# Optimization experiments

Hardware: AMD Instinct MI355X
Metric: run time of the kernel (lower is better)

## Reference

```python
import jax, jax.numpy as jnp
import numpy as np

B, T, C, H = 4096, 128, 128, 64  # T must equal BLOCK_SIZE=128, C=EMBEDDING_DIM=128


def setup_inputs() -> dict:
    key = jax.random.key(0)
    k1, k2, k3, k4, k5, k6 = jax.random.split(key, 6)
    source_embedding = jax.random.normal(k1, (B, T, C), dtype=jnp.float32)
    target_embedding = jax.random.normal(k2, (B, T, C), dtype=jnp.float32)
    # realistic padding: positions < length are valid; guarantees col 0 valid (no NaN rows)
    lengths = jax.random.randint(k3, (B,), 1, T + 1)
    pad_mask = jnp.arange(T)[None, :] < lengths[:, None]  # (B, T) bool
    Wq = jax.random.normal(k4, (C, H), dtype=jnp.float32) * 0.02
    Wk = jax.random.normal(k5, (C, H), dtype=jnp.float32) * 0.02
    Wv = jax.random.normal(k6, (C, H), dtype=jnp.float32) * 0.02
    return {"source_embedding": source_embedding, "target_embedding": target_embedding,
            "pad_mask": pad_mask, "Wq": Wq, "Wk": Wk, "Wv": Wv}


def reference(source_embedding, target_embedding, pad_mask, Wq, Wk, Wv):
    # q from target, k/v from source (cross-attention capable), bias-free projections
    q = target_embedding @ Wq   # (B, T, H)
    k = source_embedding @ Wk   # (B, T, H)
    v = source_embedding @ Wv   # (B, T, H)
    scale = k.shape[-1] ** -0.5
    wei = jnp.einsum('btd,bsd->bts', q, k) * scale  # (B, T, T)
    causal = jnp.tril(jnp.ones((T, T), dtype=bool))  # needs_future_mask=True
    mask = pad_mask[:, None, :] & causal[None, :, :]  # fuse pad + future masks
    wei = jnp.where(mask, wei, -jnp.inf)
    wei = jax.nn.softmax(wei, axis=-1)
    # dropout disabled (eval mode) for deterministic reference
    out = wei @ v  # (B, T, H)
    return out
```

## Files before the change

kernel.cpp:

```cpp
#include <hip/hip_runtime.h>
#include <stdint.h>


typedef uint32_t u32x2 __attribute__((ext_vector_type(2)));
typedef uint32_t u32x4 __attribute__((ext_vector_type(4)));
typedef float    f32x4 __attribute__((ext_vector_type(4)));
typedef __bf16   bf16x8 __attribute__((ext_vector_type(8)));

static __device__ __forceinline__ uint32_t pack2(float a, float b) {
  uint32_t ua = __builtin_bit_cast(uint32_t, a);
  uint32_t ub = __builtin_bit_cast(uint32_t, b);
  ua += 0x7FFFu + ((ua >> 16) & 1u);
  ub += 0x7FFFu + ((ub >> 16) & 1u);
  return (ua >> 16) | (ub & 0xFFFF0000u);
}
static __device__ __forceinline__ f32x4 mfma16(u32x4 a, u32x4 b, f32x4 c) {
  return __builtin_amdgcn_mfma_f32_16x16x32_bf16(
      __builtin_bit_cast(bf16x8, a), __builtin_bit_cast(bf16x8, b), c, 0, 0, 0);
}

__global__ void prep_w(const float* __restrict__ Wq, const float* __restrict__ Wk,
                       const float* __restrict__ Wv, const void* __restrict__ mask,
                       uint32_t* __restrict__ ws) {
  const int blk = blockIdx.x;
  const int l = threadIdx.x;
  if (blk < 48) {
    const int m  = blk >> 4;
    const int ct = (blk >> 2) & 3;
    const int ks = blk & 3;
    const float* W = (m == 0) ? Wq : ((m == 1) ? Wk : Wv);
    const int h  = ct * 16 + (l & 15);
    const int c0 = ks * 32 + (l >> 4) * 8;
    u32x4 v;
#pragma unroll
    for (int p = 0; p < 4; ++p)
      v[p] = pack2(W[(c0 + 2 * p) * 64 + h], W[(c0 + 2 * p + 1) * 64 + h]);
    ((u32x4*)ws)[blk * 64 + l] = v;
  } else {
    const uint32_t* mw = (const uint32_t*)mask;
    int fl = 0;
    for (int i = l * 16; i < l * 16 + 16; ++i) {
      uint32_t x = mw[i];
      if (x == 0x3F800000u) fl = 2;
      else if (x > 1u && fl != 2) fl = 1;
    }
#pragma unroll
    for (int off = 32; off > 0; off >>= 1) {
      int o = __shfl_down(fl, off);
      fl = (o > fl) ? o : fl;
    }
    if (l == 0) ws[12288] = (uint32_t)fl;
  }
}

__global__ __launch_bounds__(512, 4) void attn_fused(
    const float* __restrict__ src, const float* __restrict__ tgt,
    const void* __restrict__ mask, const uint32_t* __restrict__ ws,
    float* __restrict__ out) {
  __shared__ __align__(16) uint8_t lds[66048];
  uint8_t* const EMB = lds;
  uint8_t* const Qb  = lds + 16384;
  uint8_t* const Kb  = lds + 32768;
  uint8_t* const Vb  = lds + 49152;
  float*  const BIAS = (float*)(lds + 65536);

  const int b   = blockIdx.x;
  const int tid = (int)threadIdx.x;
  const int l   = tid & 63;
  const int w   = tid >> 6;
  const int l15 = l & 15;
  const int g4  = l >> 4;
  const int ct  = w & 3;
  const int sg  = (w >> 2) * 2;

  const u32x4* wsv = (const u32x4*)ws;
  const int mflag = (int)ws[12288];
  const float* const srcb = src + (size_t)b * 16384;
  const float* const tgtb = tgt + (size_t)b * 16384;

  u32x4 wk[4], wv[4], wq[4];
#pragma unroll
  for (int ks = 0; ks < 4; ++ks) {
    wk[ks] = wsv[((4 + ct) * 4 + ks) * 64 + l];
    wv[ks] = wsv[((8 + ct) * 4 + ks) * 64 + l];
  }

  f32x4 pf[4];
  auto stage_load = [&](const float* gbase) {
#pragma unroll
    for (int p = 0; p < 4; ++p)
      pf[p] = *(const f32x4*)(gbase + tid * 4 + p * 2048);
  };
  auto stage_write = [&]() {
#pragma unroll
    for (int p = 0; p < 4; ++p) {
      const int c   = tid + p * 512;
      const int row = c >> 5;
      const int cc  = c & 31;
      u32x2 d = { pack2(pf[p][0], pf[p][1]), pack2(pf[p][2], pf[p][3]) };
      *(u32x2*)(EMB + (row << 8) + ((((cc >> 1) ^ (row & 7))) << 4) + ((cc & 1) << 3)) = d;
    }
  };

  auto projKV = [&](int half) {
#pragma unroll
    for (int i = 0; i < 2; ++i) {
      const int st  = sg + i;
      const int row = st * 16 + l15;
      f32x4 cK = {0, 0, 0, 0}, cV = {0, 0, 0, 0};
#pragma unroll
      for (int ks = 0; ks < 4; ++ks) {
        u32x4 e = *(const u32x4*)(EMB + (row << 8) + ((((ks * 4 + g4) ^ (row & 7))) << 4));
        cK = mfma16(wk[ks], e, cK);
        cV = mfma16(e, wv[ks], cV);
      }
      const int s  = half * 64 + st * 16 + l15;
      const int h0 = ct * 16 + g4 * 4;
      u32x2 dk = { pack2(cK[0], cK[1]), pack2(cK[2], cK[3]) };
      *(u32x2*)(Kb + (s << 7) + ((((h0 >> 3) ^ (s & 7))) << 4) + ((h0 & 7) << 1)) = dk;
      const int s0 = half * 64 + st * 16 + g4 * 4;
      const int h  = ct * 16 + l15;
      u32x2 dv = { pack2(cV[0], cV[1]), pack2(cV[2], cV[3]) };
      *(u32x2*)(Vb + (h << 8) + ((((s0 >> 3) ^ (h & 7))) << 4) + ((s0 & 7) << 1)) = dv;
    }
  };
  auto projQ = [&](int half) {
#pragma unroll
    for (int i = 0; i < 2; ++i) {
      const int st  = sg + i;
      const int row = st * 16 + l15;
      f32x4 cQ = {0, 0, 0, 0};
#pragma unroll
      for (int ks = 0; ks < 4; ++ks) {
        u32x4 e = *(const u32x4*)(EMB + (row << 8) + ((((ks * 4 + g4) ^ (row & 7))) << 4));
        cQ = mfma16(wq[ks], e, cQ);
      }
      const int t  = half * 64 + st * 16 + l15;
      const int h0 = ct * 16 + g4 * 4;
      u32x2 dq = { pack2(cQ[0], cQ[1]), pack2(cQ[2], cQ[3]) };
      *(u32x2*)(Qb + (t << 7) + ((((h0 >> 3) ^ (t & 7))) << 4) + ((h0 & 7) << 1)) = dq;
    }
  };

  stage_load(srcb);
  float biasv = 0.0f;
  if (tid < 128) {
    bool valid;
    if (mflag == 1)      valid = ((const uint8_t*)mask)[b * 128 + tid] != 0;
    else if (mflag == 0) valid = ((const int*)mask)[b * 128 + tid] != 0;
    else                 valid = ((const float*)mask)[b * 128 + tid] != 0.0f;
    biasv = valid ? 0.0f : -1e30f;
  }
  stage_write();
  if (tid < 128) BIAS[tid] = biasv;
  __syncthreads();
  stage_load(srcb + 8192);
  projKV(0);
  __syncthreads();
  stage_write();
  __syncthreads();
  stage_load(tgtb);
  projKV(1);
#pragma unroll
  for (int ks = 0; ks < 4; ++ks)
    wq[ks] = wsv[(ct * 4 + ks) * 64 + l];
  __syncthreads();
  stage_write();
  __syncthreads();
  stage_load(tgtb + 8192);
  projQ(0);
  __syncthreads();
  stage_write();
  __syncthreads();
  projQ(1);
  __syncthreads();

  const int tq = 16 * w + l15;
  u32x4 qf0 = *(const u32x4*)(Qb + (tq << 7) + (((g4 ^ (tq & 7))) << 4));
  u32x4 qf1 = *(const u32x4*)(Qb + (tq << 7) + ((((4 + g4) ^ (tq & 7))) << 4));

  f32x4 sacc[8];
#pragma unroll
  for (int mt = 0; mt < 8; ++mt) sacc[mt] = {0, 0, 0, 0};
#pragma unroll
  for (int mt = 0; mt < 8; ++mt) {
    const int srow = mt * 16 + l15;
    u32x4 k0 = *(const u32x4*)(Kb + (srow << 7) + (((g4 ^ (srow & 7))) << 4));
    u32x4 k1 = *(const u32x4*)(Kb + (srow << 7) + ((((4 + g4) ^ (srow & 7))) << 4));
    sacc[mt] = mfma16(k0, qf0, sacc[mt]);
    sacc[mt] = mfma16(k1, qf1, sacc[mt]);
  }

  float m = -3.0e38f;
#pragma unroll
  for (int mt = 0; mt < 8; ++mt) {
    f32x4 b4 = *(const f32x4*)(BIAS + mt * 16 + g4 * 4);
#pragma unroll
    for (int r = 0; r < 4; ++r) {
      float v = sacc[mt][r] * 0.125f + b4[r];
      sacc[mt][r] = v;
      m = fmaxf(m, v);
    }
  }
  m = fmaxf(m, __shfl_xor(m, 16));
  m = fmaxf(m, __shfl_xor(m, 32));
  float sum = 0.0f;
#pragma unroll
  for (int mt = 0; mt < 8; ++mt) {
#pragma unroll
    for (int r = 0; r < 4; ++r) {
      const int s = mt * 16 + g4 * 4 + r;
      float p = __expf(sacc[mt][r] - m);
      p = (s <= tq) ? p : 0.0f;
      sacc[mt][r] = p;
      sum += p;
    }
  }
  sum += __shfl_xor(sum, 16);
  sum += __shfl_xor(sum, 32);
  const float inv = 1.0f / sum;

  uint8_t* const Pr = (l15 < 8) ? (EMB + w * 2048 + l15 * 256)
                                : (Qb + w * 2048 + (l15 - 8) * 256);
#pragma unroll
  for (int mt = 0; mt < 8; ++mt) {
    u32x2 d = { pack2(sacc[mt][0], sacc[mt][1]), pack2(sacc[mt][2], sacc[mt][3]) };
    const int c = mt * 2 + (g4 >> 1);
    *(u32x2*)(Pr + (((c ^ l15)) << 4) + ((g4 & 1) << 3)) = d;
  }
  __syncthreads();

  f32x4 oacc[4];
#pragma unroll
  for (int vt = 0; vt < 4; ++vt) oacc[vt] = {0, 0, 0, 0};
#pragma unroll
  for (int ks = 0; ks < 4; ++ks) {
    u32x4 pb = *(const u32x4*)(Pr + ((((ks * 4 + g4) ^ l15)) << 4));
#pragma unroll
    for (int vt = 0; vt < 4; ++vt) {
      const int vrow = vt * 16 + l15;
      u32x4 vf = *(const u32x4*)(Vb + (vrow << 8) + ((((ks * 4 + g4) ^ (vrow & 7))) << 4));
      oacc[vt] = mfma16(vf, pb, oacc[vt]);
    }
  }

  float* const ob = out + (size_t)b * 8192 + (size_t)tq * 64;
#pragma unroll
  for (int vt = 0; vt < 4; ++vt) {
    f32x4 o = { oacc[vt][0] * inv, oacc[vt][1] * inv,
                oacc[vt][2] * inv, oacc[vt][3] * inv };
    *(f32x4*)(ob + vt * 16 + g4 * 4) = o;
  }
}

extern "C" void kernel_launch(void* const* d_in, const int* in_sizes, int n_in,
                              void* d_out, int out_size, void* d_ws, size_t ws_size,
                              hipStream_t stream) {
  const float* src = (const float*)d_in[0];
  const float* tgt = (const float*)d_in[1];
  const void*  msk = d_in[2];
  const float* Wq  = (const float*)d_in[3];
  const float* Wk  = (const float*)d_in[4];
  const float* Wv  = (const float*)d_in[5];
  uint32_t* ws = (uint32_t*)d_ws;
  float* out = (float*)d_out;
  const int B = in_sizes[0] / (128 * 128);

  hipLaunchKernelGGL(prep_w, dim3(49), dim3(64), 0, stream, Wq, Wk, Wv, msk, ws);
  hipLaunchKernelGGL(attn_fused, dim3(B), dim3(512), 0, stream,
                     src, tgt, msk, ws, out);
}
```

Measured before the change: 144.8 us.

## Keep Q and P in registers via lane shuffles, drop Q LDS buffer

Each wave now projects Q for its own 16 query rows entirely in registers and feeds it to QK^T through cross-lane shuffles instead of staging it in an LDS buffer. The softmax probabilities are likewise rearranged with shuffles rather than written to LDS, which removes one barrier and the Q buffer. LDS per block drops from about 66KB to about 49KB, and launch bounds are raised so more blocks can be resident per CU. s_setprio is also wrapped around the MFMA loops. In exchange there are many more shuffle instructions, and the higher occupancy target may force register spills.

```diff
diff --git a/kernel.cpp b/kernel.cpp
--- a/kernel.cpp
+++ b/kernel.cpp
@@ -53,16 +53,15 @@
   }
 }
 
-__global__ __launch_bounds__(512, 4) void attn_fused(
+__global__ __launch_bounds__(512, 6) void attn_fused(
     const float* __restrict__ src, const float* __restrict__ tgt,
     const void* __restrict__ mask, const uint32_t* __restrict__ ws,
     float* __restrict__ out) {
-  __shared__ __align__(16) uint8_t lds[66048];
+  __shared__ __align__(16) uint8_t lds[49664];
   uint8_t* const EMB = lds;
-  uint8_t* const Qb  = lds + 16384;
-  uint8_t* const Kb  = lds + 32768;
-  uint8_t* const Vb  = lds + 49152;
-  float*  const BIAS = (float*)(lds + 65536);
+  uint8_t* const Kb  = lds + 16384;
+  uint8_t* const Vb  = lds + 32768;
+  float*  const BIAS = (float*)(lds + 49152);
 
   const int b   = blockIdx.x;
   const int tid = (int)threadIdx.x;
@@ -78,7 +77,7 @@
   const float* const srcb = src + (size_t)b * 16384;
   const float* const tgtb = tgt + (size_t)b * 16384;
 
-  u32x4 wk[4], wv[4], wq[4];
+  u32x4 wk[4], wv[4];
 #pragma unroll
   for (int ks = 0; ks < 4; ++ks) {
     wk[ks] = wsv[((4 + ct) * 4 + ks) * 64 + l];
@@ -124,22 +123,23 @@
       *(u32x2*)(Vb + (h << 8) + ((((s0 >> 3) ^ (h & 7))) << 4) + ((s0 & 7) << 1)) = dv;
     }
   };
-  auto projQ = [&](int half) {
-#pragma unroll
-    for (int i = 0; i < 2; ++i) {
-      const int st  = sg + i;
-      const int row = st * 16 + l15;
-      f32x4 cQ = {0, 0, 0, 0};
-#pragma unroll
-      for (int ks = 0; ks < 4; ++ks) {
-        u32x4 e = *(const u32x4*)(EMB + (row << 8) + ((((ks * 4 + g4) ^ (row & 7))) << 4));
-        cQ = mfma16(wq[ks], e, cQ);
-      }
-      const int t  = half * 64 + st * 16 + l15;
-      const int h0 = ct * 16 + g4 * 4;
-      u32x2 dq = { pack2(cQ[0], cQ[1]), pack2(cQ[2], cQ[3]) };
-      *(u32x2*)(Qb + (t << 7) + ((((h0 >> 3) ^ (t & 7))) << 4) + ((h0 & 7) << 1)) = dq;
-    }
+
+  uint32_t qp[8];
+  auto projQ_own = [&]() {
+    const int row = (w & 3) * 16 + l15;
+    f32x4 c0 = {0,0,0,0}, c1 = {0,0,0,0}, c2 = {0,0,0,0}, c3 = {0,0,0,0};
+#pragma unroll
+    for (int ks = 0; ks < 4; ++ks) {
+      u32x4 e = *(const u32x4*)(EMB + (row << 8) + ((((ks * 4 + g4) ^ (row & 7))) << 4));
+      c0 = mfma16(wsv[(0  + ks) * 64 + l], e, c0);
+      c1 = mfma16(wsv[(4  + ks) * 64 + l], e, c1);
+      c2 = mfma16(wsv[(8  + ks) * 64 + l], e, c2);
+      c3 = mfma16(wsv[(12 + ks) * 64 + l], e, c3);
+    }
+    qp[0] = pack2(c0[0], c0[1]); qp[1] = pack2(c0[2], c0[3]);
+    qp[2] = pack2(c1[0], c1[1]); qp[3] = pack2(c1[2], c1[3]);
+    qp[4] = pack2(c2[0], c2[1]); qp[5] = pack2(c2[2], c2[3]);
+    qp[6] = pack2(c3[0], c3[1]); qp[7] = pack2(c3[2], c3[3]);
   };
 
   stage_load(srcb);
@@ -161,35 +161,51 @@
   __syncthreads();
   stage_load(tgtb);
   projKV(1);
-#pragma unroll
-  for (int ks = 0; ks < 4; ++ks)
-    wq[ks] = wsv[(ct * 4 + ks) * 64 + l];
   __syncthreads();
   stage_write();
   __syncthreads();
   stage_load(tgtb + 8192);
-  projQ(0);
-  __syncthreads();
-  stage_write();
-  __syncthreads();
-  projQ(1);
-  __syncthreads();
+  if (w < 4) projQ_own();
+  __syncthreads();
+  stage_write();
+  __syncthreads();
+  if (w >= 4) projQ_own();
+
+  const int hi2 = g4 >> 1;
+  const int sA  = ((g4 & 1) * 2) * 16 + l15;
+  const int sB  = sA + 16;
+
+  u32x4 qB[2];
+#pragma unroll
+  for (int ks = 0; ks < 2; ++ks) {
+    uint32_t a0 = (uint32_t)__shfl((int)qp[4 * ks + 0], sA);
+    uint32_t a1 = (uint32_t)__shfl((int)qp[4 * ks + 1], sA);
+    uint32_t a2 = (uint32_t)__shfl((int)qp[4 * ks + 2], sA);
+    uint32_t a3 = (uint32_t)__shfl((int)qp[4 * ks + 3], sA);
+    uint32_t b0 = (uint32_t)__shfl((int)qp[4 * ks + 0], sB);
+    uint32_t b1 = (uint32_t)__shfl((int)qp[4 * ks + 1], sB);
+    uint32_t b2 = (uint32_t)__shfl((int)qp[4 * ks + 2], sB);
+    uint32_t b3 = (uint32_t)__shfl((int)qp[4 * ks + 3], sB);
+    qB[ks][0] = hi2 ? a2 : a0;
+    qB[ks][1] = hi2 ? a3 : a1;
+    qB[ks][2] = hi2 ? b2 : b0;
+    qB[ks][3] = hi2 ? b3 : b1;
+  }
 
   const int tq = 16 * w + l15;
-  u32x4 qf0 = *(const u32x4*)(Qb + (tq << 7) + (((g4 ^ (tq & 7))) << 4));
-  u32x4 qf1 = *(const u32x4*)(Qb + (tq << 7) + ((((4 + g4) ^ (tq & 7))) << 4));
-
   f32x4 sacc[8];
 #pragma unroll
   for (int mt = 0; mt < 8; ++mt) sacc[mt] = {0, 0, 0, 0};
+  __builtin_amdgcn_s_setprio(1);
 #pragma unroll
   for (int mt = 0; mt < 8; ++mt) {
     const int srow = mt * 16 + l15;
     u32x4 k0 = *(const u32x4*)(Kb + (srow << 7) + (((g4 ^ (srow & 7))) << 4));
     u32x4 k1 = *(const u32x4*)(Kb + (srow << 7) + ((((4 + g4) ^ (srow & 7))) << 4));
-    sacc[mt] = mfma16(k0, qf0, sacc[mt]);
-    sacc[mt] = mfma16(k1, qf1, sacc[mt]);
-  }
+    sacc[mt] = mfma16(k0, qB[0], sacc[mt]);
+    sacc[mt] = mfma16(k1, qB[1], sacc[mt]);
+  }
+  __builtin_amdgcn_s_setprio(0);
 
   float m = -3.0e38f;
 #pragma unroll
@@ -220,22 +236,32 @@
   sum += __shfl_xor(sum, 32);
   const float inv = 1.0f / sum;
 
-  uint8_t* const Pr = (l15 < 8) ? (EMB + w * 2048 + l15 * 256)
-                                : (Qb + w * 2048 + (l15 - 8) * 256);
-#pragma unroll
-  for (int mt = 0; mt < 8; ++mt) {
-    u32x2 d = { pack2(sacc[mt][0], sacc[mt][1]), pack2(sacc[mt][2], sacc[mt][3]) };
-    const int c = mt * 2 + (g4 >> 1);
-    *(u32x2*)(Pr + (((c ^ l15)) << 4) + ((g4 & 1) << 3)) = d;
-  }
-  __syncthreads();
+  uint32_t sp[16];
+#pragma unroll
+  for (int mt = 0; mt < 8; ++mt) {
+    sp[2 * mt]     = pack2(sacc[mt][0], sacc[mt][1]);
+    sp[2 * mt + 1] = pack2(sacc[mt][2], sacc[mt][3]);
+  }
 
   f32x4 oacc[4];
 #pragma unroll
   for (int vt = 0; vt < 4; ++vt) oacc[vt] = {0, 0, 0, 0};
+  __builtin_amdgcn_s_setprio(1);
 #pragma unroll
   for (int ks = 0; ks < 4; ++ks) {
-    u32x4 pb = *(const u32x4*)(Pr + ((((ks * 4 + g4) ^ l15)) << 4));
+    uint32_t a0 = (uint32_t)__shfl((int)sp[4 * ks + 0], sA);
+    uint32_t a1 = (uint32_t)__shfl((int)sp[4 * ks + 1], sA);
+    uint32_t a2 = (uint32_t)__shfl((int)sp[4 * ks + 2], sA);
+    uint32_t a3 = (uint32_t)__shfl((int)sp[4 * ks + 3], sA);
+    uint32_t b0 = (uint32_t)__shfl((int)sp[4 * ks + 0], sB);
+    uint32_t b1 = (uint32_t)__shfl((int)sp[4 * ks + 1], sB);
+    uint32_t b2 = (uint32_t)__shfl((int)sp[4 * ks + 2], sB);
+    uint32_t b3 = (uint32_t)__shfl((int)sp[4 * ks + 3], sB);
+    u32x4 pb;
+    pb[0] = hi2 ? a2 : a0;
+    pb[1] = hi2 ? a3 : a1;
+    pb[2] = hi2 ? b2 : b0;
+    pb[3] = hi2 ? b3 : b1;
 #pragma unroll
     for (int vt = 0; vt < 4; ++vt) {
       const int vrow = vt * 16 + l15;
@@ -243,6 +269,7 @@
       oacc[vt] = mfma16(vf, pb, oacc[vt]);
     }
   }
+  __builtin_amdgcn_s_setprio(0);
 
   float* const ob = out + (size_t)b * 8192 + (size_t)tq * 64;
 #pragma unroll
```

New measurement: 199.2 us. 37.6% more time.
